# Kernel tuning notes

Measured on AMD Instinct MI355X. Metric: run time of the kernel, lower is better.

## Reference

```python
import jax, jax.numpy as jnp
import numpy as np
import math

B, T, C, H = 4, 1024, 1024, 16
D = C // H
EPS = 1e-5


def layer_norm(x, w, b):
    mu = jnp.mean(x, axis=-1, keepdims=True)
    var = jnp.mean(jnp.square(x - mu), axis=-1, keepdims=True)
    return (x - mu) * jax.lax.rsqrt(var + EPS) * w + b


def setup_inputs() -> dict:
    key = jax.random.key(0)
    ks = jax.random.split(key, 8)
    s = 0.02
    return {
        "x": jax.random.normal(ks[0], (B, T, C), jnp.float32),
        "attention_mask": jnp.ones((B, T), jnp.float32),
        "ln1_w": jnp.ones((C,), jnp.float32),
        "ln1_b": jnp.zeros((C,), jnp.float32),
        "w_attn": jax.random.normal(ks[1], (C, 3 * C), jnp.float32) * s,
        "b_attn": jnp.zeros((3 * C,), jnp.float32),
        "w_proj": jax.random.normal(ks[2], (C, C), jnp.float32) * s,
        "b_proj": jnp.zeros((C,), jnp.float32),
        "threshold": jnp.float32(0.0005),  # (layer_idx+1)/n_layer * final_token_threshold
        "ln2_w": jnp.ones((C,), jnp.float32),
        "ln2_b": jnp.zeros((C,), jnp.float32),
        "w_fc": jax.random.normal(ks[3], (C, 4 * C), jnp.float32) * s,
        "b_fc": jnp.zeros((4 * C,), jnp.float32),
        "w_fc2": jax.random.normal(ks[4], (4 * C, C), jnp.float32) * s,
        "b_fc2": jnp.zeros((C,), jnp.float32),
    }


def reference(x, attention_mask, ln1_w, ln1_b, w_attn, b_attn, w_proj, b_proj,
              threshold, ln2_w, ln2_b, w_fc, b_fc, w_fc2, b_fc2):
    # ---- attention (eval mode, dropout=0; hard masking_mode) ----
    h = layer_norm(x, ln1_w, ln1_b)
    qkv = h @ w_attn + b_attn                      # (B,T,3C)
    q, k, v = jnp.split(qkv, 3, axis=-1)
    q = q.reshape(B, T, H, D).transpose(0, 2, 1, 3)  # (B,H,T,D)
    k = k.reshape(B, T, H, D).transpose(0, 2, 1, 3)
    v = v.reshape(B, T, H, D).transpose(0, 2, 1, 3)

    scale = 1.0 / math.sqrt(D)
    logits = jnp.einsum("bhqd,bhkd->bhqk", q, k) * scale  # (B,H,T,T)
    causal = jnp.tril(jnp.ones((T, T), bool))
    neg_inf = jnp.float32(-jnp.inf)
    logits = jnp.where(causal[None, None], logits, neg_inf)
    # key-side validity mask (applied in original's manual pass; mask is all-ones
    # here so flash-path y == softmax(causal logits) @ v as well)
    logits = jnp.where(attention_mask[:, None, None, :] == 0, neg_inf, logits)
    att = jax.nn.softmax(logits, axis=-1)

    y = jnp.einsum("bhqk,bhkd->bhqd", att, v)      # (B,H,T,D)
    importance = att.mean(axis=1).mean(axis=1)     # (B,T): mean over heads, then queries

    y = y.transpose(0, 2, 1, 3).reshape(B, T, C)
    x = x + (y @ w_proj + b_proj)

    # ---- hard pruning mask ----
    pruning_mask = (importance >= threshold).astype(x.dtype)
    combined_mask = attention_mask * pruning_mask
    x = x * combined_mask[:, :, None]

    # ---- MLP ----
    h2 = layer_norm(x, ln2_w, ln2_b)
    f = jax.nn.gelu(h2 @ w_fc + b_fc, approximate=False)
    x = x + (f @ w_fc2 + b_fc2)

    pruning_loss = jnp.float32(0.0)  # hard mode -> always 0
    return (x, combined_mask, pruning_loss)
```

## Files before the change

### kernel.cpp

```cpp
#include <hip/hip_runtime.h>
#include <cstdint>
#include <cstring>

typedef unsigned short u16;
typedef short bf16x8 __attribute__((ext_vector_type(8)));
typedef float f32x4 __attribute__((ext_vector_type(4)));

#define MFMA16(a,b,c) __builtin_amdgcn_mfma_f32_16x16x32_bf16(a,b,c,0,0,0)


__device__ __forceinline__ u16 f2bf(float f) {
  union { float f; uint32_t u; } un; un.f = f;
  uint32_t u = un.u;
  u += 0x7FFFu + ((u >> 16) & 1u);
  return (u16)(u >> 16);
}

__device__ __forceinline__ float bf2f(u16 h) {
  union { uint32_t u; float f; } un; un.u = ((uint32_t)h) << 16;
  return un.f;
}

__device__ __forceinline__ float gelu_fast(float v) {
  float u = 0.7978845608028654f * (v + 0.044715f * v * v * v);
  float e = __expf(2.f * u);
  float th = 1.f - __fdividef(2.f, e + 1.f);
  return 0.5f * v * (1.f + th);
}

__device__ __forceinline__ void gl_lds16(const void* g, void* l) {
  __builtin_amdgcn_global_load_lds(
      (__attribute__((address_space(1))) void*)(const_cast<void*>(g)),
      (__attribute__((address_space(3))) void*)l, 16, 0, 0);
}


__global__ __launch_bounds__(256) void transpose_all(
    const float* __restrict__ wa, const float* __restrict__ wp,
    const float* __restrict__ wf, const float* __restrict__ wf2,
    u16* __restrict__ wat, u16* __restrict__ wpt,
    u16* __restrict__ wft, u16* __restrict__ wf2t)
{
  __shared__ float tile[32][33];
  int id = blockIdx.x;
  const float* W; u16* Wt; int K, N, bx, by;
  if (id < 3072)      { W = wa;  Wt = wat;  K = 1024; N = 3072; bx = id % 96;  by = id / 96; }
  else if (id < 4096) { id -= 3072; W = wp;  Wt = wpt;  K = 1024; N = 1024; bx = id % 32; by = id / 32; }
  else if (id < 8192) { id -= 4096; W = wf;  Wt = wft;  K = 1024; N = 4096; bx = id % 128; by = id / 128; }
  else                { id -= 8192; W = wf2; Wt = wf2t; K = 4096; N = 1024; bx = id % 32; by = id / 32; }
  int kt = by * 32, nt = bx * 32;
  int tx = threadIdx.x, ty = threadIdx.y;
#pragma unroll
  for (int i = 0; i < 4; ++i)
    tile[ty + i * 8][tx] = W[(size_t)(kt + ty + i * 8) * N + nt + tx];
  __syncthreads();
#pragma unroll
  for (int i = 0; i < 4; ++i)
    Wt[(size_t)(nt + ty + i * 8) * K + kt + tx] = f2bf(tile[tx][ty + i * 8]);
}


__global__ __launch_bounds__(256) void ln_bf16(
    const float* __restrict__ x, const float* __restrict__ wt,
    const float* __restrict__ bs, u16* __restrict__ out)
{
  int row = blockIdx.x;
  int tid = threadIdx.x, lane = tid & 63, w = tid >> 6;
  const float* xr = x + (size_t)row * 1024;
  float4 v = *(const float4*)(xr + tid * 4);
  float s = v.x + v.y + v.z + v.w;
  float sq = v.x * v.x + v.y * v.y + v.z * v.z + v.w * v.w;
#pragma unroll
  for (int o = 1; o < 64; o <<= 1) { s += __shfl_xor(s, o); sq += __shfl_xor(sq, o); }
  __shared__ float ls[4], lq[4];
  if (lane == 0) { ls[w] = s; lq[w] = sq; }
  __syncthreads();
  s = ls[0] + ls[1] + ls[2] + ls[3];
  sq = lq[0] + lq[1] + lq[2] + lq[3];
  float mu = s * (1.f / 1024.f);
  float var = sq * (1.f / 1024.f) - mu * mu;
  float rstd = rsqrtf(var + 1e-5f);
  float4 wv = *(const float4*)(wt + tid * 4);
  float4 bv = *(const float4*)(bs + tid * 4);
  ushort4 o4;
  o4.x = f2bf((v.x - mu) * rstd * wv.x + bv.x);
  o4.y = f2bf((v.y - mu) * rstd * wv.y + bv.y);
  o4.z = f2bf((v.z - mu) * rstd * wv.z + bv.z);
  o4.w = f2bf((v.w - mu) * rstd * wv.w + bv.w);
  *(ushort4*)(out + (size_t)row * 1024 + tid * 4) = o4;
}


__device__ __forceinline__ void gemm_mainloop_db(
    const u16* __restrict__ Abase, const u16* __restrict__ Bbase,
    int lda, int ldb, int nIter, f32x4 acc[4][4])
{
  __shared__ __align__(16) u16 lA[2][128 * 32];
  __shared__ __align__(16) u16 lB[2][128 * 32];

  const int tid = threadIdx.x;
  const int lane = tid & 63;
  const int w = tid >> 6;
  const int wr = (w >> 1) * 64;
  const int wc = (w & 1) * 64;
  const int laneM = lane & 15;
  const int laneK = (lane >> 4) * 8;

#pragma unroll
  for (int i = 0; i < 4; ++i)
#pragma unroll
    for (int j = 0; j < 4; ++j)
      acc[i][j] = f32x4{0.f, 0.f, 0.f, 0.f};

  const int off0 = w * 1024 + lane * 16;
  const int off1 = off0 + 4096;
  const int rA0 = off0 >> 6, cb0 = off0 & 63;
  const int rA1 = off1 >> 6, cb1 = off1 & 63;

  const size_t sA = (size_t)lda * 2;
  const size_t sB = (size_t)ldb * 2;
  const char* pA0 = (const char*)Abase + (size_t)rA0 * sA + cb0;
  const char* pA1 = (const char*)Abase + (size_t)rA1 * sA + cb1;
  const char* pB0 = (const char*)Bbase + (size_t)rA0 * sB + cb0;
  const char* pB1 = (const char*)Bbase + (size_t)rA1 * sB + cb1;
  char* dA0 = (char*)&lA[0][0] + off0;
  char* dA1 = (char*)&lA[0][0] + off1;
  char* dB0 = (char*)&lB[0][0] + off0;
  char* dB1 = (char*)&lB[0][0] + off1;

  gl_lds16(pA0, dA0); gl_lds16(pA1, dA1);
  gl_lds16(pB0, dB0); gl_lds16(pB1, dB1);
  pA0 += 64; pA1 += 64; pB0 += 64; pB1 += 64;
  __syncthreads();

  for (int it = 0; it < nIter; ++it) {
    const int cur = it & 1;
    const int nb = cur ^ 1;
    if (it + 1 < nIter) {
      gl_lds16(pA0, dA0 + nb * 8192);
      gl_lds16(pA1, dA1 + nb * 8192);
      gl_lds16(pB0, dB0 + nb * 8192);
      gl_lds16(pB1, dB1 + nb * 8192);
      pA0 += 64; pA1 += 64; pB0 += 64; pB1 += 64;
    }
    const u16* aRd = &lA[cur][(wr + laneM) * 32 + laneK];
    const u16* bRd = &lB[cur][(wc + laneM) * 32 + laneK];
    bf16x8 af[4], bfr[4];
#pragma unroll
    for (int t = 0; t < 4; ++t) {
      af[t]  = *(const bf16x8*)(aRd + t * 16 * 32);
      bfr[t] = *(const bf16x8*)(bRd + t * 16 * 32);
    }
#pragma unroll
    for (int i = 0; i < 4; ++i)
#pragma unroll
      for (int j = 0; j < 4; ++j)
        acc[i][j] = MFMA16(af[i], bfr[j], acc[i][j]);
    if (it + 1 < nIter) __syncthreads();
  }
}


__global__ __launch_bounds__(256, 4) void gemm_qkv(
    const u16* __restrict__ A, const u16* __restrict__ Bt,
    const float* __restrict__ bias,
    u16* __restrict__ qo, u16* __restrict__ ko, u16* __restrict__ vo)
{
  f32x4 acc[4][4];
  int m0 = blockIdx.y * 128, n0 = blockIdx.x * 128;
  gemm_mainloop_db(A + (size_t)m0 * 1024, Bt + (size_t)n0 * 1024, 1024, 1024, 32, acc);
  const int lane = threadIdx.x & 63, w = threadIdx.x >> 6;
  const int wr = (w >> 1) * 64, wc = (w & 1) * 64;
  const int laneM = lane & 15, q4 = lane >> 4;
  const int which = (n0 >> 10);
#pragma unroll
  for (int ti = 0; ti < 4; ++ti) {
#pragma unroll
    for (int tj = 0; tj < 4; ++tj) {
      int n = n0 + wc + tj * 16 + laneM;
      int c = n & 1023;
      int hh = c >> 6, d = c & 63;
      float bval = bias[n];
      if (which == 2) {
        int m0r = m0 + wr + ti * 16 + q4 * 4;
        int b = m0r >> 10, t0 = m0r & 1023;
        ushort4 o4;
        o4.x = f2bf(acc[ti][tj][0] + bval);
        o4.y = f2bf(acc[ti][tj][1] + bval);
        o4.z = f2bf(acc[ti][tj][2] + bval);
        o4.w = f2bf(acc[ti][tj][3] + bval);
        *(ushort4*)&vo[((size_t)((b * 16 + hh) * 64 + d)) * 1024 + t0] = o4;
      } else {
        u16* dst = (which == 0) ? qo : ko;
#pragma unroll
        for (int r = 0; r < 4; ++r) {
          int m = m0 + wr + ti * 16 + q4 * 4 + r;
          int b = m >> 10, t = m & 1023;
          dst[((size_t)((b * 16 + hh) * 1024 + t)) * 64 + d] = f2bf(acc[ti][tj][r] + bval);
        }
      }
    }
  }
}

__global__ __launch_bounds__(256, 4) void gemm_proj(
    const u16* __restrict__ A, const u16* __restrict__ Bt,
    const float* __restrict__ bias, const float* __restrict__ xin,
    const float* __restrict__ maskv, float* __restrict__ x2)
{
  f32x4 acc[4][4];
  int m0 = blockIdx.y * 128, n0 = blockIdx.x * 128;
  gemm_mainloop_db(A + (size_t)m0 * 1024, Bt + (size_t)n0 * 1024, 1024, 1024, 32, acc);
  const int lane = threadIdx.x & 63, w = threadIdx.x >> 6;
  const int wr = (w >> 1) * 64, wc = (w & 1) * 64;
  const int laneM = lane & 15, q4 = lane >> 4;
#pragma unroll
  for (int ti = 0; ti < 4; ++ti) {
#pragma unroll
    for (int tj = 0; tj < 4; ++tj) {
      int n = n0 + wc + tj * 16 + laneM;
      float bval = bias[n];
#pragma unroll
      for (int r = 0; r < 4; ++r) {
        int m = m0 + wr + ti * 16 + q4 * 4 + r;
        float v = xin[(size_t)m * 1024 + n] + acc[ti][tj][r] + bval;
        x2[(size_t)m * 1024 + n] = v * maskv[m];
      }
    }
  }
}

__global__ __launch_bounds__(256, 4) void gemm_fc(
    const u16* __restrict__ A, const u16* __restrict__ Bt,
    const float* __restrict__ bias, u16* __restrict__ fo)
{
  f32x4 acc[4][4];
  int m0 = blockIdx.y * 128, n0 = blockIdx.x * 128;
  gemm_mainloop_db(A + (size_t)m0 * 1024, Bt + (size_t)n0 * 1024, 1024, 1024, 32, acc);
  const int lane = threadIdx.x & 63, w = threadIdx.x >> 6;
  const int wr = (w >> 1) * 64, wc = (w & 1) * 64;
  const int laneM = lane & 15, q4 = lane >> 4;
#pragma unroll
  for (int ti = 0; ti < 4; ++ti) {
#pragma unroll
    for (int tj = 0; tj < 4; ++tj) {
      int n = n0 + wc + tj * 16 + laneM;
      float bval = bias[n];
#pragma unroll
      for (int r = 0; r < 4; ++r) {
        int m = m0 + wr + ti * 16 + q4 * 4 + r;
        fo[(size_t)m * 4096 + n] = f2bf(gelu_fast(acc[ti][tj][r] + bval));
      }
    }
  }
}

__global__ __launch_bounds__(256, 4) void gemm_fc2_splitk(
    const u16* __restrict__ A, const u16* __restrict__ Bt,
    u16* __restrict__ pall)
{
  int id = blockIdx.x;
  int r = id & 7, j = id >> 3;
  int mt = r * 4 + (j >> 5);
  int rem = j & 31;
  int n0 = (rem & 7) * 128;
  int kz = rem >> 3;
  int m0 = mt * 128;
  f32x4 acc[4][4];
  gemm_mainloop_db(A + (size_t)m0 * 4096 + kz * 1024,
                   Bt + (size_t)n0 * 4096 + kz * 1024, 4096, 4096, 32, acc);
  u16* p = pall + (size_t)kz * 4096 * 1024;
  const int lane = threadIdx.x & 63, w = threadIdx.x >> 6;
  const int wr = (w >> 1) * 64, wc = (w & 1) * 64;
  const int laneM = lane & 15, q4 = lane >> 4;
#pragma unroll
  for (int ti = 0; ti < 4; ++ti) {
#pragma unroll
    for (int tj = 0; tj < 4; ++tj) {
      int n = n0 + wc + tj * 16 + laneM;
#pragma unroll
      for (int r2 = 0; r2 < 4; ++r2) {
        int m = m0 + wr + ti * 16 + q4 * 4 + r2;
        p[(size_t)m * 1024 + n] = f2bf(acc[ti][tj][r2]);
      }
    }
  }
}

__global__ __launch_bounds__(256) void fc2_finalize(
    const float* __restrict__ x2, const float* __restrict__ bias,
    const u16* __restrict__ pall, float* __restrict__ out)
{
  int i = blockIdx.x * 256 + threadIdx.x;
  int col4 = i & 255;
  float4 a = ((const float4*)x2)[i];
  float4 b = ((const float4*)bias)[col4];
  float s0 = a.x + b.x, s1 = a.y + b.y, s2 = a.z + b.z, s3 = a.w + b.w;
#pragma unroll
  for (int z = 0; z < 4; ++z) {
    ushort4 u = ((const ushort4*)(pall + (size_t)z * 4194304))[i];
    s0 += bf2f(u.x); s1 += bf2f(u.y); s2 += bf2f(u.z); s3 += bf2f(u.w);
  }
  float4 o; o.x = s0; o.y = s1; o.z = s2; o.w = s3;
  ((float4*)out)[i] = o;
}


__global__ __launch_bounds__(512) void attn_fwd(
    const u16* __restrict__ qb, const u16* __restrict__ kb, const u16* __restrict__ vtb,
    u16* __restrict__ yb, float* __restrict__ part)
{
  const int id = blockIdx.x;
  const int slot = (id & 7) ^ ((id >> 8) & 1);
  const int qbi = (slot & 1) ? (slot >> 1) : (7 - (slot >> 1));
  const int bh = id >> 3;
  const int b = bh >> 4, h = bh & 15;

  const int tid = threadIdx.x, lane = tid & 63, w = tid >> 6;
  const int q0 = qbi * 128;
  const int laneM = lane & 15, q4 = lane >> 4;
  const float scale = 0.125f;

  __shared__ __align__(16) u16 lK[2][64 * 72];
  __shared__ __align__(16) u16 lV[2][64 * 72];
  __shared__ __align__(16) u16 lP[8][16 * 72];
  __shared__ float part_s[1024];

  part_s[tid] = 0.f;
  part_s[tid + 512] = 0.f;

  bf16x8 qf[2];
  {
    const u16* qrow = qb + ((size_t)(bh * 1024 + q0 + w * 16 + laneM)) * 64 + q4 * 8;
    qf[0] = *(const bf16x8*)qrow;
    qf[1] = *(const bf16x8*)(qrow + 32);
  }

  const int nkt = 2 * qbi + 2;
  const int srow = tid >> 3;
  const int scol = (tid & 7) * 8;
  const u16* kbase = kb + (size_t)bh * 65536;
  const u16* vbase = vtb + (size_t)bh * 65536;

  float lrow[4] = {0.f, 0.f, 0.f, 0.f};
  {
    uint4 pk = *(const uint4*)(kbase + (size_t)srow * 64 + scol);
    *(uint4*)&lK[0][srow * 72 + scol] = pk;
    __syncthreads();
    for (int kt = 0; kt < nkt; ++kt) {
      const int cur = kt & 1;
      if (kt + 1 < nkt)
        pk = *(const uint4*)(kbase + (size_t)((kt + 1) * 64 + srow) * 64 + scol);
#pragma unroll
      for (int tj = 0; tj < 4; ++tj) {
        const u16* kp = &lK[cur][(tj * 16 + laneM) * 72 + q4 * 8];
        bf16x8 k0 = *(const bf16x8*)kp;
        bf16x8 k1 = *(const bf16x8*)(kp + 32);
        f32x4 z = {0.f, 0.f, 0.f, 0.f};
        z = MFMA16(qf[0], k0, z);
        z = MFMA16(qf[1], k1, z);
        int kc = kt * 64 + tj * 16 + laneM;
#pragma unroll
        for (int r = 0; r < 4; ++r) {
          int qg = q0 + w * 16 + q4 * 4 + r;
          lrow[r] += (kc <= qg) ? __expf(z[r] * scale) : 0.f;
        }
      }
      if (kt + 1 < nkt) *(uint4*)&lK[cur ^ 1][srow * 72 + scol] = pk;
      __syncthreads();
    }
  }
  float linv[4];
#pragma unroll
  for (int r = 0; r < 4; ++r) {
    float s = lrow[r];
    s += __shfl_xor(s, 1); s += __shfl_xor(s, 2);
    s += __shfl_xor(s, 4); s += __shfl_xor(s, 8);
    linv[r] = 1.f / s;
  }

  f32x4 o_[4];
#pragma unroll
  for (int dt = 0; dt < 4; ++dt) o_[dt] = f32x4{0.f, 0.f, 0.f, 0.f};

  {
    uint4 pk = *(const uint4*)(kbase + (size_t)srow * 64 + scol);
    uint4 pv = *(const uint4*)(vbase + (size_t)srow * 1024 + scol);
    *(uint4*)&lK[0][srow * 72 + scol] = pk;
    *(uint4*)&lV[0][srow * 72 + scol] = pv;
    __syncthreads();
    for (int kt = 0; kt < nkt; ++kt) {
      const int cur = kt & 1;
      if (kt + 1 < nkt) {
        pk = *(const uint4*)(kbase + (size_t)((kt + 1) * 64 + srow) * 64 + scol);
        pv = *(const uint4*)(vbase + (size_t)srow * 1024 + (kt + 1) * 64 + scol);
      }
      u16* lPw = &lP[w][0];
#pragma unroll
      for (int tj = 0; tj < 4; ++tj) {
        const u16* kp = &lK[cur][(tj * 16 + laneM) * 72 + q4 * 8];
        bf16x8 k0 = *(const bf16x8*)kp;
        bf16x8 k1 = *(const bf16x8*)(kp + 32);
        f32x4 z = {0.f, 0.f, 0.f, 0.f};
        z = MFMA16(qf[0], k0, z);
        z = MFMA16(qf[1], k1, z);
        int kc = kt * 64 + tj * 16 + laneM;
        float cs = 0.f;
#pragma unroll
        for (int r = 0; r < 4; ++r) {
          int qg = q0 + w * 16 + q4 * 4 + r;
          float pvf = (kc <= qg) ? __expf(z[r] * scale) * linv[r] : 0.f;
          cs += pvf;
          lPw[(q4 * 4 + r) * 72 + tj * 16 + laneM] = f2bf(pvf);
        }
        cs += __shfl_xor(cs, 16);
        cs += __shfl_xor(cs, 32);
        if (lane < 16) atomicAdd(&part_s[kt * 64 + tj * 16 + lane], cs);
      }
#pragma unroll
      for (int ss = 0; ss < 2; ++ss) {
        bf16x8 pf = *(const bf16x8*)&lP[w][laneM * 72 + ss * 32 + q4 * 8];
#pragma unroll
        for (int dt = 0; dt < 4; ++dt) {
          bf16x8 vf = *(const bf16x8*)&lV[cur][(dt * 16 + laneM) * 72 + ss * 32 + q4 * 8];
          o_[dt] = MFMA16(pf, vf, o_[dt]);
        }
      }
      if (kt + 1 < nkt) {
        *(uint4*)&lK[cur ^ 1][srow * 72 + scol] = pk;
        *(uint4*)&lV[cur ^ 1][srow * 72 + scol] = pv;
      }
      __syncthreads();
    }
  }

  const int kmax = nkt * 64;
  for (int i = tid; i < kmax; i += 512)
    atomicAdd(&part[(size_t)bh * 1024 + i], part_s[i]);

#pragma unroll
  for (int dt = 0; dt < 4; ++dt)
#pragma unroll
    for (int r = 0; r < 4; ++r) {
      int qg = q0 + w * 16 + q4 * 4 + r;
      yb[((size_t)(b * 1024 + qg)) * 1024 + h * 64 + dt * 16 + laneM] = f2bf(o_[dt][r]);
    }
}


__global__ __launch_bounds__(256) void finalize_mask(
    const float* __restrict__ part, const float* __restrict__ amask,
    const float* __restrict__ thr, float* __restrict__ mask_ws,
    float* __restrict__ out_mask, float* __restrict__ out_loss)
{
  int i = blockIdx.x * 256 + threadIdx.x;
  if (i >= 4096) return;
  int b = i >> 10;
  int t = i & 1023;
  float s = 0.f;
#pragma unroll
  for (int hh = 0; hh < 16; ++hh) s += part[(size_t)(b * 16 + hh) * 1024 + t];
  float imp = s * (1.0f / 16384.0f);
  float mv = (imp >= thr[0]) ? amask[i] : 0.f;
  mask_ws[i] = mv;
  out_mask[i] = mv;
  if (i == 0) out_loss[0] = 0.f;
}


extern "C" void kernel_launch(void* const* d_in, const int* in_sizes, int n_in,
                              void* d_out, int out_size, void* d_ws, size_t ws_size,
                              hipStream_t stream) {
  const float* x      = (const float*)d_in[0];
  const float* amask  = (const float*)d_in[1];
  const float* ln1w   = (const float*)d_in[2];
  const float* ln1b   = (const float*)d_in[3];
  const float* w_attn = (const float*)d_in[4];
  const float* b_attn = (const float*)d_in[5];
  const float* w_proj = (const float*)d_in[6];
  const float* b_proj = (const float*)d_in[7];
  const float* thr    = (const float*)d_in[8];
  const float* ln2w   = (const float*)d_in[9];
  const float* ln2b   = (const float*)d_in[10];
  const float* w_fc   = (const float*)d_in[11];
  const float* b_fc   = (const float*)d_in[12];
  const float* w_fc2  = (const float*)d_in[13];
  const float* b_fc2  = (const float*)d_in[14];
  float* out = (float*)d_out;

  char* ws = (char*)d_ws;
  size_t off = 0;
  auto alloc = [&](size_t bytes) -> char* {
    char* p = ws + off;
    off += (bytes + 255) & ~(size_t)255;
    return p;
  };
  u16* wattnT = (u16*)alloc((size_t)3072 * 1024 * 2);
  u16* wprojT = (u16*)alloc((size_t)1024 * 1024 * 2);
  u16* wfcT   = (u16*)alloc((size_t)4096 * 1024 * 2);
  u16* wfc2T  = (u16*)alloc((size_t)1024 * 4096 * 2);
  u16* hbuf   = (u16*)alloc((size_t)4096 * 1024 * 2);
  u16* qbuf   = (u16*)alloc((size_t)64 * 1024 * 64 * 2);
  u16* kbuf   = (u16*)alloc((size_t)64 * 1024 * 64 * 2);
  u16* vtbuf  = (u16*)alloc((size_t)64 * 64 * 1024 * 2);
  u16* ybuf   = (u16*)alloc((size_t)4096 * 1024 * 2);
  float* part = (float*)alloc((size_t)64 * 1024 * 4);
  float* maskws = (float*)alloc((size_t)4096 * 4);
  float* x2   = (float*)alloc((size_t)4096 * 1024 * 4);
  u16* h2     = (u16*)alloc((size_t)4096 * 1024 * 2);
  u16* fbuf   = (u16*)alloc((size_t)4096 * 4096 * 2);

  u16* pall = qbuf;

  transpose_all<<<12288, dim3(32, 8), 0, stream>>>(
      w_attn, w_proj, w_fc, w_fc2, wattnT, wprojT, wfcT, wfc2T);

  hipMemsetAsync(part, 0, (size_t)64 * 1024 * 4, stream);

  ln_bf16<<<4096, 256, 0, stream>>>(x, ln1w, ln1b, hbuf);

  gemm_qkv<<<dim3(24, 32), 256, 0, stream>>>(hbuf, wattnT, b_attn, qbuf, kbuf, vtbuf);

  attn_fwd<<<512, 512, 0, stream>>>(qbuf, kbuf, vtbuf, ybuf, part);

  finalize_mask<<<16, 256, 0, stream>>>(part, amask, thr, maskws,
                                        out + 4194304, out + 4198400);

  gemm_proj<<<dim3(8, 32), 256, 0, stream>>>(ybuf, wprojT, b_proj, x, maskws, x2);

  ln_bf16<<<4096, 256, 0, stream>>>(x2, ln2w, ln2b, h2);

  gemm_fc<<<dim3(32, 32), 256, 0, stream>>>(h2, wfcT, b_fc, fbuf);

  gemm_fc2_splitk<<<1024, 256, 0, stream>>>(fbuf, wfc2T, pall);

  fc2_finalize<<<4096, 256, 0, stream>>>(x2, b_fc2, pall, out);
}
```

Baseline: 348.9 us.

## Use 256x256 tiled 8-wave GEMM with 4-stage direct-to-LDS pipeline

```diff
diff --git a/kernel.cpp b/kernel.cpp
--- a/kernel.cpp
+++ b/kernel.cpp
@@ -91,6 +91,98 @@
 }
 
 
+__device__ __forceinline__ void gemm256_mainloop(
+    const char* __restrict__ Ab, const char* __restrict__ Bb,
+    size_t sA, size_t sB, int nT,
+    f32x4 acc[8][4], u16* lA, u16* lB)
+{
+  const int tid = threadIdx.x;
+  const int lane = tid & 63, w = tid >> 6;
+  const int laneM = lane & 15, q4 = lane >> 4;
+  const int wr = w >> 2, wc = w & 3;
+
+#pragma unroll
+  for (int i = 0; i < 8; ++i)
+#pragma unroll
+    for (int j = 0; j < 4; ++j)
+      acc[i][j] = f32x4{0.f, 0.f, 0.f, 0.f};
+
+  const int ch = (((tid & 3) ^ ((tid >> 3) & 3)) << 4);
+  const char* srcA0 = Ab + (size_t)(tid >> 2) * sA + ch;
+  const char* srcA1 = srcA0 + (size_t)128 * sA;
+  const char* srcB0 = Bb + (size_t)(tid >> 2) * sB + ch;
+  const char* srcB1 = srcB0 + (size_t)128 * sB;
+  char* dA0 = (char*)lA + tid * 16;
+  char* dB0 = (char*)lB + tid * 16;
+
+  const int swz = ((q4 ^ ((laneM >> 1) & 3)) << 4);
+  const char* rdA = (const char*)lA + (wr * 128 + laneM) * 64 + swz;
+  const char* rdB = (const char*)lB + (wc * 64 + laneM) * 64 + swz;
+
+#pragma unroll
+  for (int t = 0; t < 3; ++t) {
+    gl_lds16(srcA0 + t * 64, dA0 + t * 16384);
+    gl_lds16(srcA1 + t * 64, dA0 + t * 16384 + 8192);
+    gl_lds16(srcB0 + t * 64, dB0 + t * 16384);
+    gl_lds16(srcB1 + t * 64, dB0 + t * 16384 + 8192);
+  }
+  asm volatile("s_waitcnt vmcnt(8)" ::: "memory");
+  __builtin_amdgcn_s_barrier();
+  asm volatile("" ::: "memory");
+
+  for (int t = 0; t < nT; ++t) {
+    const int cb = (t & 3) << 14;
+    const int sb = ((t + 3) & 3) << 14;
+    const bool st = (t + 3) < nT;
+    const char* rA = rdA + cb;
+    const char* rB = rdB + cb;
+
+    bf16x8 aF[4], bF[4];
+#pragma unroll
+    for (int i = 0; i < 4; ++i) aF[i] = *(const bf16x8*)(rA + i * 1024);
+#pragma unroll
+    for (int i = 0; i < 4; ++i) bF[i] = *(const bf16x8*)(rB + i * 1024);
+    if (st) {
+      gl_lds16(srcA0 + (size_t)(t + 3) * 64, dA0 + sb);
+      gl_lds16(srcA1 + (size_t)(t + 3) * 64, dA0 + sb + 8192);
+    }
+    __builtin_amdgcn_s_barrier();
+    asm volatile("s_waitcnt lgkmcnt(0)" ::: "memory");
+    __builtin_amdgcn_s_setprio(1);
+#pragma unroll
+    for (int i = 0; i < 4; ++i)
+#pragma unroll
+      for (int j = 0; j < 4; ++j)
+        acc[i][j] = MFMA16(aF[i], bF[j], acc[i][j]);
+    __builtin_amdgcn_s_setprio(0);
+    __builtin_amdgcn_s_barrier();
+    asm volatile("" ::: "memory");
+
+    bf16x8 aG[4];
+#pragma unroll
+    for (int i = 0; i < 4; ++i) aG[i] = *(const bf16x8*)(rA + 4096 + i * 1024);
+    if (st) {
+      gl_lds16(srcB0 + (size_t)(t + 3) * 64, dB0 + sb);
+      gl_lds16(srcB1 + (size_t)(t + 3) * 64, dB0 + sb + 8192);
+    }
+    __builtin_amdgcn_s_barrier();
+    asm volatile("s_waitcnt lgkmcnt(0)" ::: "memory");
+    __builtin_amdgcn_s_setprio(1);
+#pragma unroll
+    for (int i = 0; i < 4; ++i)
+#pragma unroll
+      for (int j = 0; j < 4; ++j)
+        acc[4 + i][j] = MFMA16(aG[i], bF[j], acc[4 + i][j]);
+    __builtin_amdgcn_s_setprio(0);
+    if (t + 4 <= nT)      asm volatile("s_waitcnt vmcnt(8)" ::: "memory");
+    else if (t + 3 == nT) asm volatile("s_waitcnt vmcnt(4)" ::: "memory");
+    else                  asm volatile("s_waitcnt vmcnt(0)" ::: "memory");
+    __builtin_amdgcn_s_barrier();
+    asm volatile("" ::: "memory");
+  }
+}
+
+
 __device__ __forceinline__ void gemm_mainloop_db(
     const u16* __restrict__ Abase, const u16* __restrict__ Bbase,
     int lda, int ldb, int nIter, f32x4 acc[4][4])
@@ -161,10 +253,60 @@
 }
 
 
-__global__ __launch_bounds__(256, 4) void gemm_qkv(
+__global__ __launch_bounds__(512, 2) void gemm_qkv(
     const u16* __restrict__ A, const u16* __restrict__ Bt,
     const float* __restrict__ bias,
     u16* __restrict__ qo, u16* __restrict__ ko, u16* __restrict__ vo)
+{
+  __shared__ __align__(16) u16 lA[4][8192];
+  __shared__ __align__(16) u16 lB[4][8192];
+  const int id = blockIdx.x;
+  const int my = ((id & 7) << 1) | ((id >> 3) & 1);
+  const int nx = id >> 4;
+  const int m0 = my * 256, n0 = nx * 256;
+  f32x4 acc[8][4];
+  gemm256_mainloop((const char*)(A + (size_t)m0 * 1024),
+                   (const char*)(Bt + (size_t)n0 * 1024),
+                   2048, 2048, 32, acc, &lA[0][0], &lB[0][0]);
+
+  const int lane = threadIdx.x & 63, w = threadIdx.x >> 6;
+  const int wr = w >> 2, wc = w & 3;
+  const int laneM = lane & 15, q4 = lane >> 4;
+  const int which = n0 >> 10;
+#pragma unroll
+  for (int fr = 0; fr < 8; ++fr) {
+#pragma unroll
+    for (int fc = 0; fc < 4; ++fc) {
+      int n = n0 + wc * 64 + fc * 16 + laneM;
+      int c = n & 1023;
+      int hh = c >> 6, d = c & 63;
+      float bval = bias[n];
+      if (which == 2) {
+        int m0r = m0 + wr * 128 + fr * 16 + q4 * 4;
+        int b = m0r >> 10, t0 = m0r & 1023;
+        ushort4 o4;
+        o4.x = f2bf(acc[fr][fc][0] + bval);
+        o4.y = f2bf(acc[fr][fc][1] + bval);
+        o4.z = f2bf(acc[fr][fc][2] + bval);
+        o4.w = f2bf(acc[fr][fc][3] + bval);
+        *(ushort4*)&vo[((size_t)((b * 16 + hh) * 64 + d)) * 1024 + t0] = o4;
+      } else {
+        u16* dst = (which == 0) ? qo : ko;
+#pragma unroll
+        for (int r = 0; r < 4; ++r) {
+          int m = m0 + wr * 128 + fr * 16 + q4 * 4 + r;
+          int b = m >> 10, t = m & 1023;
+          dst[((size_t)((b * 16 + hh) * 1024 + t)) * 64 + d] = f2bf(acc[fr][fc][r] + bval);
+        }
+      }
+    }
+  }
+}
+
+__global__ __launch_bounds__(256, 4) void gemm_proj(
+    const u16* __restrict__ A, const u16* __restrict__ Bt,
+    const float* __restrict__ bias, const float* __restrict__ xin,
+    const float* __restrict__ maskv, float* __restrict__ x2)
 {
   f32x4 acc[4][4];
   int m0 = blockIdx.y * 128, n0 = blockIdx.x * 128;
@@ -172,48 +314,6 @@
   const int lane = threadIdx.x & 63, w = threadIdx.x >> 6;
   const int wr = (w >> 1) * 64, wc = (w & 1) * 64;
   const int laneM = lane & 15, q4 = lane >> 4;
-  const int which = (n0 >> 10);
-#pragma unroll
-  for (int ti = 0; ti < 4; ++ti) {
-#pragma unroll
-    for (int tj = 0; tj < 4; ++tj) {
-      int n = n0 + wc + tj * 16 + laneM;
-      int c = n & 1023;
-      int hh = c >> 6, d = c & 63;
-      float bval = bias[n];
-      if (which == 2) {
-        int m0r = m0 + wr + ti * 16 + q4 * 4;
-        int b = m0r >> 10, t0 = m0r & 1023;
-        ushort4 o4;
-        o4.x = f2bf(acc[ti][tj][0] + bval);
-        o4.y = f2bf(acc[ti][tj][1] + bval);
-        o4.z = f2bf(acc[ti][tj][2] + bval);
-        o4.w = f2bf(acc[ti][tj][3] + bval);
-        *(ushort4*)&vo[((size_t)((b * 16 + hh) * 64 + d)) * 1024 + t0] = o4;
-      } else {
-        u16* dst = (which == 0) ? qo : ko;
-#pragma unroll
-        for (int r = 0; r < 4; ++r) {
-          int m = m0 + wr + ti * 16 + q4 * 4 + r;
-          int b = m >> 10, t = m & 1023;
-          dst[((size_t)((b * 16 + hh) * 1024 + t)) * 64 + d] = f2bf(acc[ti][tj][r] + bval);
-        }
-      }
-    }
-  }
-}
-
-__global__ __launch_bounds__(256, 4) void gemm_proj(
-    const u16* __restrict__ A, const u16* __restrict__ Bt,
-    const float* __restrict__ bias, const float* __restrict__ xin,
-    const float* __restrict__ maskv, float* __restrict__ x2)
-{
-  f32x4 acc[4][4];
-  int m0 = blockIdx.y * 128, n0 = blockIdx.x * 128;
-  gemm_mainloop_db(A + (size_t)m0 * 1024, Bt + (size_t)n0 * 1024, 1024, 1024, 32, acc);
-  const int lane = threadIdx.x & 63, w = threadIdx.x >> 6;
-  const int wr = (w >> 1) * 64, wc = (w & 1) * 64;
-  const int laneM = lane & 15, q4 = lane >> 4;
 #pragma unroll
   for (int ti = 0; ti < 4; ++ti) {
 #pragma unroll
@@ -230,58 +330,69 @@
   }
 }
 
-__global__ __launch_bounds__(256, 4) void gemm_fc(
+__global__ __launch_bounds__(512, 2) void gemm_fc(
     const u16* __restrict__ A, const u16* __restrict__ Bt,
     const float* __restrict__ bias, u16* __restrict__ fo)
 {
-  f32x4 acc[4][4];
-  int m0 = blockIdx.y * 128, n0 = blockIdx.x * 128;
-  gemm_mainloop_db(A + (size_t)m0 * 1024, Bt + (size_t)n0 * 1024, 1024, 1024, 32, acc);
+  __shared__ __align__(16) u16 lA[4][8192];
+  __shared__ __align__(16) u16 lB[4][8192];
+  const int id = blockIdx.x;
+  const int my = ((id & 7) << 1) | ((id >> 3) & 1);
+  const int nx = id >> 4;
+  const int m0 = my * 256, n0 = nx * 256;
+  f32x4 acc[8][4];
+  gemm256_mainloop((const char*)(A + (size_t)m0 * 1024),
+                   (const char*)(Bt + (size_t)n0 * 1024),
+                   2048, 2048, 32, acc, &lA[0][0], &lB[0][0]);
+
   const int lane = threadIdx.x & 63, w = threadIdx.x >> 6;
-  const int wr = (w >> 1) * 64, wc = (w & 1) * 64;
+  const int wr = w >> 2, wc = w & 3;
   const int laneM = lane & 15, q4 = lane >> 4;
 #pragma unroll
-  for (int ti = 0; ti < 4; ++ti) {
-#pragma unroll
-    for (int tj = 0; tj < 4; ++tj) {
-      int n = n0 + wc + tj * 16 + laneM;
+  for (int fr = 0; fr < 8; ++fr) {
+#pragma unroll
+    for (int fc = 0; fc < 4; ++fc) {
+      int n = n0 + wc * 64 + fc * 16 + laneM;
       float bval = bias[n];
 #pragma unroll
       for (int r = 0; r < 4; ++r) {
-        int m = m0 + wr + ti * 16 + q4 * 4 + r;
-        fo[(size_t)m * 4096 + n] = f2bf(gelu_fast(acc[ti][tj][r] + bval));
-      }
-    }
-  }
-}
-
-__global__ __launch_bounds__(256, 4) void gemm_fc2_splitk(
+        int m = m0 + wr * 128 + fr * 16 + q4 * 4 + r;
+        fo[(size_t)m * 4096 + n] = f2bf(gelu_fast(acc[fr][fc][r] + bval));
+      }
+    }
+  }
+}
+
+__global__ __launch_bounds__(512, 2) void gemm_fc2_splitk(
     const u16* __restrict__ A, const u16* __restrict__ Bt,
     u16* __restrict__ pall)
 {
-  int id = blockIdx.x;
-  int r = id & 7, j = id >> 3;
-  int mt = r * 4 + (j >> 5);
-  int rem = j & 31;
-  int n0 = (rem & 7) * 128;
-  int kz = rem >> 3;
-  int m0 = mt * 128;
-  f32x4 acc[4][4];
-  gemm_mainloop_db(A + (size_t)m0 * 4096 + kz * 1024,
-                   Bt + (size_t)n0 * 4096 + kz * 1024, 4096, 4096, 32, acc);
+  __shared__ __align__(16) u16 lA[4][8192];
+  __shared__ __align__(16) u16 lB[4][8192];
+  const int id = blockIdx.x;
+  const int cmb = (id & 7) | (((id >> 7) & 1) << 3);
+  const int mt = (id >> 3) & 15;
+  const int n0 = (cmb & 3) * 256;
+  const int kz = cmb >> 2;
+  const int m0 = mt * 256;
+  f32x4 acc[8][4];
+  gemm256_mainloop((const char*)(A + (size_t)m0 * 4096 + kz * 1024),
+                   (const char*)(Bt + (size_t)n0 * 4096 + kz * 1024),
+                   8192, 8192, 32, acc, &lA[0][0], &lB[0][0]);
+
   u16* p = pall + (size_t)kz * 4096 * 1024;
   const int lane = threadIdx.x & 63, w = threadIdx.x >> 6;
-  const int wr = (w >> 1) * 64, wc = (w & 1) * 64;
+  const int wr = w >> 2, wc = w & 3;
   const int laneM = lane & 15, q4 = lane >> 4;
 #pragma unroll
-  for (int ti = 0; ti < 4; ++ti) {
-#pragma unroll
-    for (int tj = 0; tj < 4; ++tj) {
-      int n = n0 + wc + tj * 16 + laneM;
-#pragma unroll
-      for (int r2 = 0; r2 < 4; ++r2) {
-        int m = m0 + wr + ti * 16 + q4 * 4 + r2;
-        p[(size_t)m * 1024 + n] = f2bf(acc[ti][tj][r2]);
+  for (int fr = 0; fr < 8; ++fr) {
+#pragma unroll
+    for (int fc = 0; fc < 4; ++fc) {
+      int n = n0 + wc * 64 + fc * 16 + laneM;
+#pragma unroll
+      for (int r = 0; r < 4; ++r) {
+        int m = m0 + wr * 128 + fr * 16 + q4 * 4 + r;
+        p[(size_t)m * 1024 + n] = f2bf(acc[fr][fc][r]);
       }
     }
   }
@@ -519,7 +630,7 @@
 
   ln_bf16<<<4096, 256, 0, stream>>>(x, ln1w, ln1b, hbuf);
 
-  gemm_qkv<<<dim3(24, 32), 256, 0, stream>>>(hbuf, wattnT, b_attn, qbuf, kbuf, vtbuf);
+  gemm_qkv<<<192, 512, 0, stream>>>(hbuf, wattnT, b_attn, qbuf, kbuf, vtbuf);
 
   attn_fwd<<<512, 512, 0, stream>>>(qbuf, kbuf, vtbuf, ybuf, part);
 
@@ -530,9 +641,9 @@
 
   ln_bf16<<<4096, 256, 0, stream>>>(x2, ln2w, ln2b, h2);
 
-  gemm_fc<<<dim3(32, 32), 256, 0, stream>>>(h2, wfcT, b_fc, fbuf);
-
-  gemm_fc2_splitk<<<1024, 256, 0, stream>>>(fbuf, wfc2T, pall);
+  gemm_fc<<<256, 512, 0, stream>>>(h2, wfcT, b_fc, fbuf);
+
+  gemm_fc2_splitk<<<256, 512, 0, stream>>>(fbuf, wfc2T, pall);
 
   fc2_finalize<<<4096, 256, 0, stream>>>(x2, b_fc2, pall, out);
 }
```

New measurement: 354.5 us. Within noise of the previous version (+1.6%).
